# Optimization experiments

Measured on AMD Instinct MI355X. Metric: run time of the kernel, lower is better.

## Reference

```python
import jax, jax.numpy as jnp
import numpy as np

B, S, DIM = 2, 2048, 1024
H, DH = 16, 64  # num_head, head_dim


def setup_inputs() -> dict:
    key = jax.random.key(0)
    ks = jax.random.split(key, 9)
    s = 1.0 / np.sqrt(DIM)
    s2 = 1.0 / np.sqrt(H * DH)
    return {
        "X": jax.random.normal(ks[0], (B, S, DIM), dtype=jnp.float32),
        "mask": jnp.ones((B, S), dtype=jnp.float32),
        "Wq": jax.random.normal(ks[1], (DIM, H * DH), dtype=jnp.float32) * s,
        "bq": jax.random.normal(ks[2], (H * DH,), dtype=jnp.float32) * s,
        "Wk": jax.random.normal(ks[3], (DIM, H * DH), dtype=jnp.float32) * s,
        "bk": jax.random.normal(ks[4], (H * DH,), dtype=jnp.float32) * s,
        "Wv": jax.random.normal(ks[5], (DIM, H * DH), dtype=jnp.float32) * s,
        "bv": jax.random.normal(ks[6], (H * DH,), dtype=jnp.float32) * s,
        "Wo": jax.random.normal(ks[7], (H * DH, DIM), dtype=jnp.float32) * s2,
        "bo": jax.random.normal(ks[8], (DIM,), dtype=jnp.float32) * s2,
    }


def _split_heads(x):
    # [B,S,H*DH] -> [B,H,S,DH]
    return x.reshape(B, S, H, DH).transpose(0, 2, 1, 3)


def reference(X, mask, Wq, bq, Wk, bk, Wv, bv, Wo, bo):
    Q = _split_heads(X @ Wq + bq)
    K = _split_heads(X @ Wk + bk)
    V = _split_heads(X @ Wv + bv)
    # scores: [B,H,S,S]
    dot = jnp.einsum("bhqd,bhkd->bhqk", Q, K) / np.sqrt(DH).astype(np.float32)
    dot = dot - 1000000.0 * (1.0 - mask[:, None, None, :])
    attn = jax.nn.softmax(dot, axis=-1)
    ctx = jnp.einsum("bhqk,bhkd->bhqd", attn, V)
    # combine heads: [B,S,H*DH]
    ctx = ctx.transpose(0, 2, 1, 3).reshape(B, S, H * DH)
    return ctx @ Wo + bo
```

## Files before the change

kernel.cpp:

```cpp
#include <hip/hip_runtime.h>
#include <hip/hip_bf16.h>
#include <math.h>

#define BB 2
#define SS 2048
#define DIM 1024
#define NH 16
#define DH 64

typedef __bf16 bf16x8 __attribute__((ext_vector_type(8)));
typedef float f32x4 __attribute__((ext_vector_type(4)));
typedef float f32x16 __attribute__((ext_vector_type(16)));
typedef unsigned int u32x4 __attribute__((ext_vector_type(4)));

#define PENL2 (1000000.0f * 1.44269504f)

#define VMW(N) asm volatile("s_waitcnt vmcnt(" #N ")" ::: "memory")

__device__ __forceinline__ void glds16(const __hip_bfloat16* g, __hip_bfloat16* l) {
    __builtin_amdgcn_global_load_lds(
        (const __attribute__((address_space(1))) void*)g,
        (__attribute__((address_space(3))) void*)l, 16, 0, 0);
}

__device__ __forceinline__ void glds4(const float* g, float* l) {
    __builtin_amdgcn_global_load_lds(
        (const __attribute__((address_space(1))) void*)g,
        (__attribute__((address_space(3))) void*)l, 4, 0, 0);
}

__device__ __forceinline__ unsigned short f2bf(float x) {
    unsigned int u = __builtin_bit_cast(unsigned int, x);
    return (unsigned short)((u + 0x8000u) >> 16);
}

__device__ __forceinline__ unsigned int pk2bf(float a, float b) {
#if __has_builtin(__builtin_amdgcn_cvt_pk_bf16_f32)
    typedef __bf16 bf16x2 __attribute__((ext_vector_type(2)));
    bf16x2 p = __builtin_amdgcn_cvt_pk_bf16_f32(a, b);
    return __builtin_bit_cast(unsigned int, p);
#else
    return (unsigned int)f2bf(a) | ((unsigned int)f2bf(b) << 16);
#endif
}

__device__ __forceinline__ float fexp2(float x) {
#if __has_builtin(__builtin_amdgcn_exp2f)
    return __builtin_amdgcn_exp2f(x);
#else
    return exp2f(x);
#endif
}

__global__ void prep(const float* __restrict__ X,
                     const float* __restrict__ Wq, const float* __restrict__ Wk,
                     const float* __restrict__ Wv, const float* __restrict__ Wo,
                     const float* __restrict__ mask, float* __restrict__ pf,
                     __hip_bfloat16* __restrict__ T4, ushort4* __restrict__ Xbf) {
    int z = blockIdx.z;
    int t = threadIdx.x;
    if (z == 4) {
        int c = blockIdx.y * 32 + blockIdx.x;
        const float4* in = (const float4*)X;
#pragma unroll
        for (int k = 0; k < 4; ++k) {
            int i = c * 1024 + k * 256 + t;
            float4 v = in[i];
            ushort4 h;
            h.x = f2bf(v.x); h.y = f2bf(v.y); h.z = f2bf(v.z); h.w = f2bf(v.w);
            Xbf[i] = h;
        }
        if (c < 16) {
            int i = c * 256 + t;
            pf[i] = -PENL2 * (1.0f - mask[i]);
        }
        return;
    }
    const float* W = (z == 0) ? Wq : (z == 1) ? Wk : (z == 2) ? Wv : Wo;
    __hip_bfloat16* Thi = T4 + (size_t)z * DIM * DIM;
    __shared__ float tile[32][33];
    int k0 = blockIdx.x * 32, n0 = blockIdx.y * 32;
    int r = t >> 3, c = (t & 7) << 2;
    float4 v = *(const float4*)&W[(size_t)(k0 + r) * DIM + n0 + c];
    tile[r][c] = v.x; tile[r][c + 1] = v.y; tile[r][c + 2] = v.z; tile[r][c + 3] = v.w;
    __syncthreads();
    size_t base = (size_t)(n0 + r) * DIM + k0 + c;
#pragma unroll
    for (int i = 0; i < 4; ++i)
        ((unsigned short*)Thi)[base + i] = f2bf(tile[c + i][r]);
}

#define BM 128
#define BK 32
#define QSCALE (0.125f * 1.44269504f)
template <int TBN>
__global__ __launch_bounds__(512, 6) void gemm_bf(
    const __hip_bfloat16* __restrict__ A, const __hip_bfloat16* __restrict__ B,
    const float* __restrict__ b0, const float* __restrict__ b1, const float* __restrict__ b2,
    __hip_bfloat16* __restrict__ oq, __hip_bfloat16* __restrict__ ok,
    __hip_bfloat16* __restrict__ ov, float* __restrict__ of32, int mode) {
    __shared__ alignas(16) __hip_bfloat16 sA[3][BM * BK];
    __shared__ alignas(16) __hip_bfloat16 sB[3][TBN * BK];
    const int K = 1024;
    const int JF = TBN / 64;
    int tid = threadIdx.x;
    int wave = tid >> 6, lane = tid & 63, quad = lane >> 4, l16 = lane & 15;

    int nbx = gridDim.x;
    int nwg = nbx * gridDim.y;
    int bid = blockIdx.y * nbx + blockIdx.x;
    int swz = (bid & 7) * (nwg >> 3) + (bid >> 3);
    int m0 = (swz / nbx) * BM, n0 = (swz % nbx) * TBN;
    int mo = (wave >> 2) * 64, no = (wave & 3) * (TBN / 4);

    f32x4 acc[4][JF];
#pragma unroll
    for (int i = 0; i < 4; ++i)
#pragma unroll
        for (int j = 0; j < JF; ++j) acc[i][j] = (f32x4){0.f, 0.f, 0.f, 0.f};

    int ar = tid >> 2;
    int c4 = tid & 3;
    int cs = c4 ^ ((ar >> 1) & 3);
    const __hip_bfloat16* gA = A + (size_t)(m0 + ar) * K + cs * 8;
    const __hip_bfloat16* gB = B + (size_t)(n0 + ar) * K + cs * 8;
    int ldst = ar * BK + c4 * 8;
    bool stgB = (ar < TBN);

    auto STG = [&](int bb, int k0) {
        glds16(gA + k0, &sA[bb][ldst]);
        if (stgB) glds16(gB + k0, &sB[bb][ldst]);
    };

    STG(0, 0);
    STG(1, BK);
    int cur = 0;
    for (int it = 0; it < 32; ++it) {
        int k0 = it * BK;
        if (it < 30) {
            int nb = cur + 2; if (nb >= 3) nb -= 3;
            STG(nb, k0 + 2 * BK);
            if (stgB) { VMW(4); } else { VMW(2); }
        } else if (it == 30) {
            if (stgB) { VMW(2); } else { VMW(1); }
        } else {
            VMW(0);
        }
        __builtin_amdgcn_s_barrier();

        bf16x8 a_h[4], b_h[JF];
#pragma unroll
        for (int i = 0; i < 4; ++i) {
            int rr = mo + i * 16 + l16;
            int ph = quad ^ ((rr >> 1) & 3);
            a_h[i] = *(const bf16x8*)&sA[cur][rr * BK + ph * 8];
        }
#pragma unroll
        for (int j = 0; j < JF; ++j) {
            int rr = no + j * 16 + l16;
            int ph = quad ^ ((rr >> 1) & 3);
            b_h[j] = *(const bf16x8*)&sB[cur][rr * BK + ph * 8];
        }
        __builtin_amdgcn_s_setprio(1);
#pragma unroll
        for (int i = 0; i < 4; ++i)
#pragma unroll
            for (int j = 0; j < JF; ++j)
                acc[i][j] = __builtin_amdgcn_mfma_f32_16x16x32_bf16(a_h[i], b_h[j], acc[i][j], 0, 0, 0);
        __builtin_amdgcn_s_setprio(0);
        __builtin_amdgcn_s_barrier();
        cur = (cur == 2) ? 0 : cur + 1;
    }

    int which = (mode == 1) ? (n0 >> 10) : 0;
    const float* bp = (mode == 0) ? b0 : (which == 0) ? b0 : (which == 1) ? b1 : b2;
#pragma unroll
    for (int i = 0; i < 4; ++i)
#pragma unroll
        for (int j = 0; j < JF; ++j) {
            int gmb = m0 + mo + i * 16 + quad * 4;
            int gn  = n0 + no + j * 16 + l16;
            int nn  = gn & 1023;
            float bb = bp[(mode == 0) ? gn : nn];
#pragma unroll
            for (int r = 0; r < 4; ++r) {
                int gm = gmb + r;
                float v = acc[i][j][r] + bb;
                if (mode == 0) {
                    of32[(size_t)gm * 1024 + gn] = v;
                } else {
                    int b = gm >> 11, s = gm & 2047, h = nn >> 6, d = nn & 63;
                    if (which == 0)
                        ((unsigned short*)oq)[(((size_t)(b * NH + h)) * SS + s) * DH + d] = f2bf(v * QSCALE);
                    else if (which == 1)
                        ((unsigned short*)ok)[(((size_t)(b * NH + h)) * SS + s) * DH + d] = f2bf(v);
                    else
                        ((unsigned short*)ov)[(((size_t)(b * NH + h)) * DH + d) * SS + s] = f2bf(v);
                }
            }
        }
}

__global__ __launch_bounds__(256, 4) void flash_split(
        const __hip_bfloat16* __restrict__ Q,
        const __hip_bfloat16* __restrict__ K,
        const __hip_bfloat16* __restrict__ Vt,
        const float* __restrict__ pf,
        __hip_bfloat16* __restrict__ Op0, __hip_bfloat16* __restrict__ Op1,
        float* __restrict__ lp0, float* __restrict__ lp1) {
    int bidl = blockIdx.x + (blockIdx.y << 4) + (blockIdx.z << 9);
    int w = (bidl & 7) * 128 + (bidl >> 3);
    int q0 = (w & 15) * 128;
    int bh = (w >> 4) & 31;
    int z  = w >> 9;
    int b = bh >> 4, h = bh & (NH - 1);
    __hip_bfloat16* Op = z ? Op1 : Op0;
    float*          lp = z ? lp1 : lp0;
    int tid = threadIdx.x;
    int wave = tid >> 6, lane = tid & 63;
    int l31 = lane & 31, hi = lane >> 5, l7 = lane & 7;

    __shared__ alignas(16) __hip_bfloat16 sK[2][64 * 64];
    __shared__ alignas(16) __hip_bfloat16 sV[2][64 * 64];
    __shared__ alignas(16) float sPF[2][64];

    const __hip_bfloat16* Qrow = Q + ((size_t)bh * SS + q0 + wave * 32 + l31) * DH;
    bf16x8 aq[4];
#pragma unroll
    for (int d_ = 0; d_ < 4; ++d_)
        aq[d_] = *(const bf16x8*)(Qrow + d_ * 16 + 8 * hi);

    const __hip_bfloat16* Kb = K + (size_t)bh * SS * DH;
    const __hip_bfloat16* Vb = Vt + (size_t)bh * DH * SS;
    const float* pfp = pf + b * SS;

    f32x16 z16;
#pragma unroll
    for (int r = 0; r < 16; ++r) z16[r] = 0.f;
    f32x16 O[2];
    O[0] = z16; O[1] = z16;
    f32x4 ls = (f32x4){0.f, 0.f, 0.f, 0.f};

    int xo[4];
#pragma unroll
    for (int c = 0; c < 4; ++c) xo[c] = ((((c << 1) | hi) ^ l7) << 4);

    int r8 = lane >> 3, c8 = lane & 7;
    int ck = c8 ^ r8;

    const int kbeg = z * (SS / 2);
    const int NT = (SS / 2) / 64;

    auto STAGE = [&](int bb, int k0) {
#pragma unroll
        for (int cc = 0; cc < 2; ++cc) {
            int row = cc * 32 + wave * 8 + r8;
            glds16(Kb + (size_t)(k0 + row) * DH + ck * 8, &sK[bb][row * 64 + c8 * 8]);
            glds16(Vb + (size_t)row * SS + k0 + ck * 8,  &sV[bb][row * 64 + c8 * 8]);
        }
        if (wave == 0)
            glds4(pfp + k0 + lane, &sPF[bb][0]);
    };

    STAGE(0, kbeg);
    __syncthreads();
    int cur = 0;
    for (int t = 0; t < NT; ++t) {
        int k0 = kbeg + t * 64;
        if (t + 1 < NT) STAGE(cur ^ 1, k0 + 64);
#pragma unroll
        for (int tt = 0; tt < 2; ++tt) {
            const char* pK = (const char*)&sK[cur][(tt * 32 + l31) * 64];
            bf16x8 kf[4];
#pragma unroll
            for (int d_ = 0; d_ < 4; ++d_)
                kf[d_] = *(const bf16x8*)(pK + xo[d_]);
            f32x16 st;
#pragma unroll
            for (int g = 0; g < 4; ++g) {
                f32x4 pv = *(const f32x4*)&sPF[cur][32 * tt + 8 * g + 4 * hi];
#pragma unroll
                for (int j = 0; j < 4; ++j) st[4 * g + j] = pv[j];
            }
            __builtin_amdgcn_s_setprio(1);
#pragma unroll
            for (int d_ = 0; d_ < 4; ++d_)
                st = __builtin_amdgcn_mfma_f32_32x32x16_bf16(kf[d_], aq[d_], st, 0, 0, 0);
            __builtin_amdgcn_s_setprio(0);

#pragma unroll
            for (int g = 0; g < 4; ++g) {
#pragma unroll
                for (int j = 0; j < 4; ++j)
                    st[4 * g + j] = fexp2(st[4 * g + j]);
                ls[0] += st[4 * g];     ls[1] += st[4 * g + 1];
                ls[2] += st[4 * g + 2]; ls[3] += st[4 * g + 3];
            }

            unsigned int u[8];
#pragma unroll
            for (int g = 0; g < 4; ++g) {
                u[2 * g]     = pk2bf(st[4 * g],     st[4 * g + 1]);
                u[2 * g + 1] = pk2bf(st[4 * g + 2], st[4 * g + 3]);
            }

#pragma unroll
            for (int kk = 0; kk < 2; ++kk) {
                unsigned int w0 = u[4 * kk],     w2 = u[4 * kk + 2];
                unsigned int w1 = u[4 * kk + 1], w3 = u[4 * kk + 3];
                asm("v_permlane32_swap_b32 %0, %1" : "+v"(w0), "+v"(w2));
                asm("v_permlane32_swap_b32 %0, %1" : "+v"(w1), "+v"(w3));
                u32x4 paw; paw.x = w0; paw.y = w1; paw.z = w2; paw.w = w3;
                bf16x8 pa = __builtin_bit_cast(bf16x8, paw);
                int ks = 2 * tt + kk;
                __builtin_amdgcn_s_setprio(1);
#pragma unroll
                for (int dt_ = 0; dt_ < 2; ++dt_) {
                    const char* pV = (const char*)&sV[cur][(dt_ * 32 + l31) * 64];
                    bf16x8 vf = *(const bf16x8*)(pV + xo[ks]);
                    O[dt_] = __builtin_amdgcn_mfma_f32_32x32x16_bf16(pa, vf, O[dt_], 0, 0, 0);
                }
                __builtin_amdgcn_s_setprio(0);
            }
        }
        __syncthreads();
        cur ^= 1;
    }

    unsigned short* op = (unsigned short*)Op;
    int qb = q0 + wave * 32;
#pragma unroll
    for (int dt_ = 0; dt_ < 2; ++dt_)
#pragma unroll
        for (int r = 0; r < 16; ++r) {
            int qq = (r & 3) + 8 * (r >> 2) + 4 * hi;
            op[((size_t)b * SS + qb + qq) * (NH * DH) + h * DH + dt_ * 32 + l31] =
                f2bf(O[dt_][r]);
        }
    float lt = ls[0] + ls[1] + ls[2] + ls[3];
    lt += __shfl_xor(lt, 32, 64);
    if (hi == 0)
        lp[(size_t)bh * SS + qb + l31] = lt;
}

__global__ __launch_bounds__(256) void combine(
        const __hip_bfloat16* __restrict__ O1, const __hip_bfloat16* __restrict__ O2,
        const float* __restrict__ l1, const float* __restrict__ l2,
        __hip_bfloat16* __restrict__ ctx) {
    int i = blockIdx.x * 256 + threadIdx.x;
    size_t base = (size_t)i * 8;
    int row = i >> 7;
    int h   = (i >> 3) & 15;
    int b = row >> 11, s = row & 2047;
    size_t bhq = ((size_t)(b * NH + h)) * SS + s;
    float linv = 1.0f / (l1[bhq] + l2[bhq]);
    bf16x8 a = *(const bf16x8*)(O1 + base);
    bf16x8 c = *(const bf16x8*)(O2 + base);
    ushort4 o0, o1;
    o0.x = f2bf(((float)a[0] + (float)c[0]) * linv);
    o0.y = f2bf(((float)a[1] + (float)c[1]) * linv);
    o0.z = f2bf(((float)a[2] + (float)c[2]) * linv);
    o0.w = f2bf(((float)a[3] + (float)c[3]) * linv);
    o1.x = f2bf(((float)a[4] + (float)c[4]) * linv);
    o1.y = f2bf(((float)a[5] + (float)c[5]) * linv);
    o1.z = f2bf(((float)a[6] + (float)c[6]) * linv);
    o1.w = f2bf(((float)a[7] + (float)c[7]) * linv);
    ((ushort4*)(ctx + base))[0] = o0;
    ((ushort4*)(ctx + base + 4))[0] = o1;
}

extern "C" void kernel_launch(void* const* d_in, const int* in_sizes, int n_in,
                              void* d_out, int out_size, void* d_ws, size_t ws_size,
                              hipStream_t stream) {
    const float* X    = (const float*)d_in[0];
    const float* mask = (const float*)d_in[1];
    const float* Wq   = (const float*)d_in[2];
    const float* bq   = (const float*)d_in[3];
    const float* Wk   = (const float*)d_in[4];
    const float* bk   = (const float*)d_in[5];
    const float* Wv   = (const float*)d_in[6];
    const float* bv   = (const float*)d_in[7];
    const float* Wo   = (const float*)d_in[8];
    const float* bo   = (const float*)d_in[9];
    float* out = (float*)d_out;

    const size_t MB = 1u << 20;
    char* ws = (char*)d_ws;
    __hip_bfloat16* Xbf = (__hip_bfloat16*)(ws);
    __hip_bfloat16* Op0 = (__hip_bfloat16*)(ws + 8 * MB);
    __hip_bfloat16* Wt4 = (__hip_bfloat16*)(ws + 16 * MB);
    float*          lp0 = (float*)(ws + 24 * MB);
    float*          lp1 = (float*)(ws + 25 * MB);
    float*          pf  = (float*)(ws + 26 * MB);
    __hip_bfloat16* Qw  = (__hip_bfloat16*)(ws + 32 * MB);
    __hip_bfloat16* Kw  = (__hip_bfloat16*)(ws + 40 * MB);
    __hip_bfloat16* Vt  = (__hip_bfloat16*)(ws + 48 * MB);
    __hip_bfloat16* Op1 = (__hip_bfloat16*)(ws + 56 * MB);
    __hip_bfloat16* Wot = Wt4 + (size_t)3 * DIM * DIM;

    dim3 pgrd(32, 32, 5);
    prep<<<pgrd, 256, 0, stream>>>(X, Wq, Wk, Wv, Wo, mask, pf, Wt4, (ushort4*)Xbf);

    dim3 qkvgrd(3 * DIM / 128, (BB * SS) / BM);
    gemm_bf<128><<<qkvgrd, 512, 0, stream>>>(Xbf, Wt4, bq, bk, bv,
                                             Qw, Kw, Vt, nullptr, 1);

    dim3 agrd(SS / 128, BB * NH, 2);
    flash_split<<<agrd, 256, 0, stream>>>(Qw, Kw, Vt, pf, Op0, Op1, lp0, lp1);

    combine<<<dim3(2048), 256, 0, stream>>>(Op0, Op1, lp0, lp1, Xbf);

    dim3 ogrd(DIM / 64, (BB * SS) / BM);
    gemm_bf<64><<<ogrd, 512, 0, stream>>>(Xbf, Wot, bo, nullptr, nullptr,
                                          nullptr, nullptr, nullptr, out, 0);
}
```

Baseline: 205.9 us.

## Fuse split-attention combine into output projection GEMM A-tile loading

Removes the separate combine kernel and instead merges the two partial attention outputs and normalizes by the summed softmax denominators while staging A tiles in a new output-projection GEMM. This is meant to eliminate one kernel launch and the write and re-read of the bf16 context buffer. In exchange, A tiles are loaded through registers rather than direct global-to-LDS copies, and each tile of 1024 columns is read from two buffers, which may add latency inside the GEMM's main loop.

```diff
diff --git a/kernel.cpp b/kernel.cpp
--- a/kernel.cpp
+++ b/kernel.cpp
@@ -49,6 +49,14 @@
     return __builtin_amdgcn_exp2f(x);
 #else
     return exp2f(x);
+#endif
+}
+
+__device__ __forceinline__ float frcp(float x) {
+#if __has_builtin(__builtin_amdgcn_rcpf)
+    return __builtin_amdgcn_rcpf(x);
+#else
+    return 1.0f / x;
 #endif
 }
 
@@ -199,6 +207,115 @@
                 }
             }
         }
+}
+
+__global__ __launch_bounds__(512, 4) void gemm_of(
+    const __hip_bfloat16* __restrict__ O1, const __hip_bfloat16* __restrict__ O2,
+    const float* __restrict__ l1, const float* __restrict__ l2,
+    const __hip_bfloat16* __restrict__ Bw,
+    const float* __restrict__ bias, float* __restrict__ out) {
+    __shared__ alignas(16) __hip_bfloat16 sA[2][BM * BK];
+    __shared__ alignas(16) __hip_bfloat16 sB[2][64 * BK];
+    int tid = threadIdx.x;
+    int wave = tid >> 6, lane = tid & 63, quad = lane >> 4, l16 = lane & 15;
+
+    int nbx = gridDim.x;
+    int nwg = nbx * gridDim.y;
+    int bid = blockIdx.y * nbx + blockIdx.x;
+    int swz = (bid & 7) * (nwg >> 3) + (bid >> 3);
+    int m0 = (swz / nbx) * BM, n0 = (swz % nbx) * 64;
+    int mo = (wave >> 2) * 64, no = (wave & 3) * 16;
+
+    f32x4 acc[4];
+#pragma unroll
+    for (int i = 0; i < 4; ++i) acc[i] = (f32x4){0.f, 0.f, 0.f, 0.f};
+
+    int ar = tid >> 2;
+    int c4 = tid & 3;
+    int cs = c4 ^ ((ar >> 1) & 3);
+    int m  = m0 + ar;
+    int bq16 = (m >> 11) * NH;
+    int sq   = m & 2047;
+    const __hip_bfloat16* gO1 = O1 + (size_t)m * 1024 + cs * 8;
+    const __hip_bfloat16* gO2 = O2 + (size_t)m * 1024 + cs * 8;
+    const __hip_bfloat16* gB  = Bw + (size_t)(n0 + ar) * 1024 + cs * 8;
+    int ldst = ar * BK + c4 * 8;
+    bool stgB = (ar < 64);
+
+    bf16x8 n1 = *(const bf16x8*)(gO1);
+    bf16x8 n2 = *(const bf16x8*)(gO2);
+    float  nl = l1[(size_t)bq16 * SS + sq] + l2[(size_t)bq16 * SS + sq];
+    if (stgB) glds16(gB, &sB[0][ldst]);
+    {
+        float linv = frcp(nl);
+        unsigned int p0 = pk2bf(((float)n1[0] + (float)n2[0]) * linv,
+                                ((float)n1[1] + (float)n2[1]) * linv);
+        unsigned int p1 = pk2bf(((float)n1[2] + (float)n2[2]) * linv,
+                                ((float)n1[3] + (float)n2[3]) * linv);
+        unsigned int p2 = pk2bf(((float)n1[4] + (float)n2[4]) * linv,
+                                ((float)n1[5] + (float)n2[5]) * linv);
+        unsigned int p3 = pk2bf(((float)n1[6] + (float)n2[6]) * linv,
+                                ((float)n1[7] + (float)n2[7]) * linv);
+        u32x4 pw; pw.x = p0; pw.y = p1; pw.z = p2; pw.w = p3;
+        *(bf16x8*)&sA[0][ldst] = __builtin_bit_cast(bf16x8, pw);
+    }
+    __syncthreads();
+
+    int cur = 0;
+    for (int it = 0; it < 32; ++it) {
+        if (it < 31) {
+            int k0n = (it + 1) * BK;
+            n1 = *(const bf16x8*)(gO1 + k0n);
+            n2 = *(const bf16x8*)(gO2 + k0n);
+            size_t bhq = (size_t)(bq16 + (k0n >> 6)) * SS + sq;
+            nl = l1[bhq] + l2[bhq];
+            if (stgB) glds16(gB + k0n, &sB[cur ^ 1][ldst]);
+        }
+
+        bf16x8 a_h[4], b_h;
+#pragma unroll
+        for (int i = 0; i < 4; ++i) {
+            int rr = mo + i * 16 + l16;
+            int ph = quad ^ ((rr >> 1) & 3);
+            a_h[i] = *(const bf16x8*)&sA[cur][rr * BK + ph * 8];
+        }
+        {
+            int rr = no + l16;
+            int ph = quad ^ ((rr >> 1) & 3);
+            b_h = *(const bf16x8*)&sB[cur][rr * BK + ph * 8];
+        }
+        __builtin_amdgcn_s_setprio(1);
+#pragma unroll
+        for (int i = 0; i < 4; ++i)
+            acc[i] = __builtin_amdgcn_mfma_f32_16x16x32_bf16(a_h[i], b_h, acc[i], 0, 0, 0);
+        __builtin_amdgcn_s_setprio(0);
+
+        if (it < 31) {
+            float linv = frcp(nl);
+            unsigned int p0 = pk2bf(((float)n1[0] + (float)n2[0]) * linv,
+                                    ((float)n1[1] + (float)n2[1]) * linv);
+            unsigned int p1 = pk2bf(((float)n1[2] + (float)n2[2]) * linv,
+                                    ((float)n1[3] + (float)n2[3]) * linv);
+            unsigned int p2 = pk2bf(((float)n1[4] + (float)n2[4]) * linv,
+                                    ((float)n1[5] + (float)n2[5]) * linv);
+            unsigned int p3 = pk2bf(((float)n1[6] + (float)n2[6]) * linv,
+                                    ((float)n1[7] + (float)n2[7]) * linv);
+            u32x4 pw; pw.x = p0; pw.y = p1; pw.z = p2; pw.w = p3;
+            *(bf16x8*)&sA[cur ^ 1][ldst] = __builtin_bit_cast(bf16x8, pw);
+        }
+        __syncthreads();
+        cur ^= 1;
+    }
+
+#pragma unroll
+    for (int i = 0; i < 4; ++i) {
+        int gmb = m0 + mo + i * 16 + quad * 4;
+        int gn  = n0 + no + l16;
+        float bb = bias[gn];
+#pragma unroll
+        for (int r = 0; r < 4; ++r)
+            out[(size_t)(gmb + r) * 1024 + gn] = acc[i][r] + bb;
+    }
 }
 
 __global__ __launch_bounds__(256, 4) void flash_split(
@@ -343,32 +460,6 @@
         lp[(size_t)bh * SS + qb + l31] = lt;
 }
 
-__global__ __launch_bounds__(256) void combine(
-        const __hip_bfloat16* __restrict__ O1, const __hip_bfloat16* __restrict__ O2,
-        const float* __restrict__ l1, const float* __restrict__ l2,
-        __hip_bfloat16* __restrict__ ctx) {
-    int i = blockIdx.x * 256 + threadIdx.x;
-    size_t base = (size_t)i * 8;
-    int row = i >> 7;
-    int h   = (i >> 3) & 15;
-    int b = row >> 11, s = row & 2047;
-    size_t bhq = ((size_t)(b * NH + h)) * SS + s;
-    float linv = 1.0f / (l1[bhq] + l2[bhq]);
-    bf16x8 a = *(const bf16x8*)(O1 + base);
-    bf16x8 c = *(const bf16x8*)(O2 + base);
-    ushort4 o0, o1;
-    o0.x = f2bf(((float)a[0] + (float)c[0]) * linv);
-    o0.y = f2bf(((float)a[1] + (float)c[1]) * linv);
-    o0.z = f2bf(((float)a[2] + (float)c[2]) * linv);
-    o0.w = f2bf(((float)a[3] + (float)c[3]) * linv);
-    o1.x = f2bf(((float)a[4] + (float)c[4]) * linv);
-    o1.y = f2bf(((float)a[5] + (float)c[5]) * linv);
-    o1.z = f2bf(((float)a[6] + (float)c[6]) * linv);
-    o1.w = f2bf(((float)a[7] + (float)c[7]) * linv);
-    ((ushort4*)(ctx + base))[0] = o0;
-    ((ushort4*)(ctx + base + 4))[0] = o1;
-}
-
 extern "C" void kernel_launch(void* const* d_in, const int* in_sizes, int n_in,
                               void* d_out, int out_size, void* d_ws, size_t ws_size,
                               hipStream_t stream) {
@@ -408,9 +499,6 @@
     dim3 agrd(SS / 128, BB * NH, 2);
     flash_split<<<agrd, 256, 0, stream>>>(Qw, Kw, Vt, pf, Op0, Op1, lp0, lp1);
 
-    combine<<<dim3(2048), 256, 0, stream>>>(Op0, Op1, lp0, lp1, Xbf);
-
     dim3 ogrd(DIM / 64, (BB * SS) / BM);
-    gemm_bf<64><<<ogrd, 512, 0, stream>>>(Xbf, Wot, bo, nullptr, nullptr,
-                                          nullptr, nullptr, nullptr, out, 0);
-}
+    gemm_of<<<ogrd, 512, 0, stream>>>(Op0, Op1, lp0, lp1, Wot, bo, out);
+}
```

Result: slower. 211.6 us (+2.8%).
